# Kernel optimization log

Hardware: AMD Instinct MI355X
Metric: run time of the kernel (lower is better)

Reference implementation:

```python
import jax, jax.numpy as jnp
import numpy as np

B, T, C, H = 2, 2048, 1024, 16
D = C // H  # head_dim = 64


def wheel_softmax(scores):
    """Wheel-arithmetic softmax: total division, bot (0/0) positions -> 0.
    Rows that are entirely -inf yield sum==0 -> bot -> filled with 0.0,
    matching wheel_out.to_numpy_safe(bot_fill=0.0, inf_fill=0.0)."""
    m = jnp.max(scores, axis=-1, keepdims=True)
    safe_m = jnp.where(jnp.isfinite(m), m, 0.0)
    e = jnp.exp(scores - safe_m)          # -inf entries -> 0
    z = jnp.sum(e, axis=-1, keepdims=True)
    ok = z > 0
    return jnp.where(ok, e / jnp.where(ok, z, 1.0), 0.0)


def setup_inputs() -> dict:
    key = jax.random.key(0)
    ks = jax.random.split(key, 12)
    s = 1.0 / np.sqrt(C)
    inp = {
        "query": jax.random.normal(ks[0], (B, T, C), jnp.float32),
        "key": jax.random.normal(ks[1], (B, T, C), jnp.float32),
        "value": jax.random.normal(ks[2], (B, T, C), jnp.float32),
        "q_w": jax.random.normal(ks[3], (C, C), jnp.float32) * s,
        "q_b": jax.random.normal(ks[4], (C,), jnp.float32) * 0.01,
        "k_w": jax.random.normal(ks[5], (C, C), jnp.float32) * s,
        "k_b": jax.random.normal(ks[6], (C,), jnp.float32) * 0.01,
        "v_w": jax.random.normal(ks[7], (C, C), jnp.float32) * s,
        "v_b": jax.random.normal(ks[8], (C,), jnp.float32) * 0.01,
        "o_w": jax.random.normal(ks[9], (C, C), jnp.float32) * s,
        "o_b": jax.random.normal(ks[10], (C,), jnp.float32) * 0.01,
        "key_padding_mask": jax.random.randint(ks[11], (B, T), 0, 2).astype(bool),
    }
    return inp


def reference(query, key, value, q_w, q_b, k_w, k_b, v_w, v_b, o_w, o_b, key_padding_mask):
    scale = D ** -0.5
    def proj(x, w, b):
        # nn.Linear: x @ w.T + b ; reshape to [B,H,T,D]
        y = jnp.einsum("btc,oc->bto", x, w) + b
        return y.reshape(B, T, H, D).transpose(0, 2, 1, 3)
    Q = proj(query, q_w, q_b)
    K = proj(key, k_w, k_b)
    V = proj(value, v_w, v_b)
    scores = jnp.einsum("bhqd,bhkd->bhqk", Q, K) * scale
    scores = jnp.where(key_padding_mask[:, None, None, :], -jnp.inf, scores)
    weights = wheel_softmax(scores)  # dropout=0 -> identity
    out = jnp.einsum("bhqk,bhkd->bhqd", weights, V)
    out = out.transpose(0, 2, 1, 3).reshape(B, T, C)
    out = jnp.einsum("btc,oc->bto", out, o_w) + o_b
    return (out, weights)
```

## Files before the change

### kernel.cpp

```cpp
#include <hip/hip_runtime.h>
#include <math.h>


typedef _Float16 f16;
typedef _Float16 f16x2 __attribute__((ext_vector_type(2)));
typedef _Float16 f16x4 __attribute__((ext_vector_type(4)));
typedef _Float16 f16x8 __attribute__((ext_vector_type(8)));
typedef float  f32x2  __attribute__((ext_vector_type(2)));
typedef float  f32x4  __attribute__((ext_vector_type(4)));

#define MFMAH(a, b, c)  __builtin_amdgcn_mfma_f32_16x16x32_f16((a), (b), (c), 0, 0, 0)

__device__ __forceinline__ void gload16(void* lds, const void* g) {
  __builtin_amdgcn_global_load_lds((__attribute__((address_space(1))) void*)(g),
                                   (__attribute__((address_space(3))) void*)(lds),
                                   16, 0, 0);
}

__global__ __launch_bounds__(256) void conv_f16(const float* __restrict__ q, const float* __restrict__ k,
                                                const float* __restrict__ v, const float* __restrict__ qw,
                                                const float* __restrict__ kw, const float* __restrict__ vw,
                                                const float* __restrict__ ow, f16* __restrict__ xf) {
  long long i = ((long long)blockIdx.x * 256 + threadIdx.x) * 4;
  const float* src;
  long long off;
  if (i < 4194304)       { src = q;  off = 0; }
  else if (i < 8388608)  { src = k;  off = 4194304; }
  else if (i < 12582912) { src = v;  off = 8388608; }
  else if (i < 13631488) { src = qw; off = 12582912; }
  else if (i < 14680064) { src = kw; off = 13631488; }
  else if (i < 15728640) { src = vw; off = 14680064; }
  else                   { src = ow; off = 15728640; }
  f32x4 val = *(const f32x4*)(src + (i - off));
  f16x4 h;
#pragma unroll
  for (int r = 0; r < 4; ++r) h[r] = (f16)val[r];
  *(f16x4*)(xf + i) = h;
}

__device__ __forceinline__ void stage_tile(f16* lds, const f16* g, int row0, int kc, int tid) {
#pragma unroll
  for (int j = 0; j < 2; ++j) {
    int chunk = j * 256 + tid;
    int r = chunk >> 2, cpos = chunk & 3;
    int csrc = cpos ^ ((r >> 1) & 3);
    gload16((char*)lds + chunk * 16,
            (const char*)(g + (size_t)(row0 + r) * 1024 + kc) + csrc * 16);
  }
}

__device__ __forceinline__ f16x8 frag_ld(const f16* lds, int row, int g) {
  int pos = g ^ ((row >> 1) & 3);
  return *(const f16x8*)((const char*)lds + row * 64 + pos * 16);
}

__device__ __forceinline__ void gemm_core(const f16* A, const f16* X, int o0, int t0, int tid,
                                          f16* sA, f16* sB, f32x4 acc[4][4]) {
  int wid = tid >> 6, lane = tid & 63;
  int wm = wid >> 1, wn = wid & 1, g = lane >> 4, r15 = lane & 15;
  for (int kc = 0; kc < 1024; kc += 32) {
    __syncthreads();
    stage_tile(sA, A, o0, kc, tid);
    stage_tile(sB, X, t0, kc, tid);
    __syncthreads();
    f16x8 a[4], x[4];
#pragma unroll
    for (int f = 0; f < 4; ++f) {
      a[f] = frag_ld(sA, wm * 64 + f * 16 + r15, g);
      x[f] = frag_ld(sB, wn * 64 + f * 16 + r15, g);
    }
#pragma unroll
    for (int fm = 0; fm < 4; ++fm)
#pragma unroll
      for (int fn = 0; fn < 4; ++fn)
        acc[fm][fn] = MFMAH(a[fm], x[fn], acc[fm][fn]);
  }
}

__global__ __launch_bounds__(256) void gemm_qk(const f16* __restrict__ xf,
                                               const float* __restrict__ q_b, const float* __restrict__ k_b,
                                               f16* __restrict__ Qf, f16* __restrict__ Kf) {
  __shared__ f16 sA[4096], sB[4096];
  int z = blockIdx.z;
  const f16* A = xf + (z ? 13631488 : 12582912);
  const f16* X = xf + (z ? 4194304 : 0);
  const float* bias = z ? k_b : q_b;
  f16* Yf = z ? Kf : Qf;
  float scale = z ? 1.0f : 0.125f;
  int tid = threadIdx.x;
  int o0 = blockIdx.x * 128, t0 = blockIdx.y * 128;
  int wid = tid >> 6, lane = tid & 63;
  int wm = wid >> 1, wn = wid & 1, g = lane >> 4, r15 = lane & 15;
  f32x4 acc[4][4] = {};
  gemm_core(A, X, o0, t0, tid, sA, sB, acc);
#pragma unroll
  for (int fm = 0; fm < 4; ++fm)
#pragma unroll
    for (int fn = 0; fn < 4; ++fn) {
      int ob = o0 + wm * 64 + fm * 16 + 4 * g;
      int t  = t0 + wn * 64 + fn * 16 + r15;
      int bb = t >> 11, tl = t & 2047, hh = ob >> 6, dd = ob & 63;
      size_t base = (((size_t)bb * 16 + hh) * 2048 + tl) * 64 + dd;
      f16x4 vh;
#pragma unroll
      for (int r = 0; r < 4; ++r)
        vh[r] = (f16)((acc[fm][fn][r] + bias[ob + r]) * scale);
      *(f16x4*)(Yf + base) = vh;
    }
}

__global__ __launch_bounds__(256) void gemm_v(const f16* __restrict__ xf,
                                              const float* __restrict__ bias, f16* __restrict__ VT2) {
  __shared__ f16 sA[4096], sB[4096];
  const f16* X = xf + 8388608;
  const f16* W = xf + 14680064;
  int tid = threadIdx.x;
  int t0 = blockIdx.x * 128, o0 = blockIdx.y * 128;
  int wid = tid >> 6, lane = tid & 63;
  int wm = wid >> 1, wn = wid & 1, g = lane >> 4, r15 = lane & 15;
  f32x4 acc[4][4] = {};
  gemm_core(X, W, t0, o0, tid, sA, sB, acc);
#pragma unroll
  for (int fm = 0; fm < 4; ++fm)
#pragma unroll
    for (int fn = 0; fn < 4; ++fn) {
      int tb = t0 + wm * 64 + fm * 16 + 4 * g;
      int o  = o0 + wn * 64 + fn * 16 + r15;
      int bb = tb >> 11, tl = tb & 2047, hh = o >> 6, dd = o & 63;
      int ch = tl >> 5, c = tl & 31;
      int slotbase = (c < 16) ? ((c >> 2) << 3) : ((((c - 16) >> 2) << 3) + 4);
      float bo = bias[o];
      f16x4 v4;
#pragma unroll
      for (int r = 0; r < 4; ++r) v4[r] = (f16)(acc[fm][fn][r] + bo);
      *(f16x4*)(VT2 + ((((size_t)bb * 16 + hh) * 64 + ch) * 64 + dd) * 32 + slotbase) = v4;
    }
}

__global__ __launch_bounds__(256) void gemm_o(const f16* __restrict__ xf, const f16* __restrict__ Abuf,
                                              const float* __restrict__ o_b, float* __restrict__ OutF) {
  __shared__ f16 sA[4096], sB[4096];
  const f16* A = xf + 15728640;
  int tid = threadIdx.x;
  int o0 = blockIdx.x * 128, t0 = blockIdx.y * 128;
  int wid = tid >> 6, lane = tid & 63;
  int wm = wid >> 1, wn = wid & 1, g = lane >> 4, r15 = lane & 15;
  f32x4 acc[4][4] = {};
  gemm_core(A, Abuf, o0, t0, tid, sA, sB, acc);
#pragma unroll
  for (int fm = 0; fm < 4; ++fm)
#pragma unroll
    for (int fn = 0; fn < 4; ++fn) {
      int ob = o0 + wm * 64 + fm * 16 + 4 * g;
      int t  = t0 + wn * 64 + fn * 16 + r15;
      f32x4 v;
#pragma unroll
      for (int r = 0; r < 4; ++r) v[r] = acc[fm][fn][r] + o_b[ob + r];
      *(f32x4*)(OutF + (size_t)t * 1024 + ob) = v;
    }
}

__global__ __launch_bounds__(512, 4) void attn_kernel(
    const f16* __restrict__ Qf, const f16* __restrict__ Kf,
    const f16* __restrict__ VT2, const int* __restrict__ mask,
    float* __restrict__ wout, f16* __restrict__ Abuf) {
  __shared__ f16 kstage[8][2][1024];
  __shared__ float pvbuf[8 * 1088];
  __shared__ float ps[128];
  __shared__ float rz[16];
  int tid = threadIdx.x;
  int wid = tid >> 6, lane = tid & 63;
  int g = lane >> 4, r15 = lane & 15;
  int qt = blockIdx.x & 127, bh = blockIdx.x >> 7;
  int b = bh >> 4, h = bh & 15;
  int q0 = qt * 16;

  const f16* qp = Qf + ((size_t)bh * 2048 + q0 + r15) * 64 + 8 * g;
  f16x8 qh0 = *(const f16x8*)(qp);
  f16x8 qh1 = *(const f16x8*)(qp + 32);

  const int* mp = mask + b * 2048 + wid * 256 + 4 * g;
  unsigned long long mb = 0;
#pragma unroll
  for (int t = 0; t < 16; ++t) {
    int4 ma = *(const int4*)(mp + t * 16);
    mb |= ((ma.x ? 1ull : 0ull) << (4 * t)) | ((ma.y ? 1ull : 0ull) << (4 * t + 1)) |
          ((ma.z ? 1ull : 0ull) << (4 * t + 2)) | ((ma.w ? 1ull : 0ull) << (4 * t + 3));
  }

  f16* kb0 = &kstage[wid][0][0];
  f16* kb1 = &kstage[wid][1][0];
  const f16* ksrcA = Kf + ((size_t)bh * 2048 + wid * 256 + (lane >> 3)) * 64 +
                     (((lane & 7) ^ ((lane >> 3) & 7)) * 8);
  const f16* ksrcB = ksrcA + 8 * 64;

  gload16(kb0, ksrcA);
  gload16(kb0 + 512, ksrcB);
  gload16(kb1, ksrcA + 1024);
  gload16(kb1 + 512, ksrcB + 1024);

  float psum = 0.f;
  f16x4 p16[16];
  int key = r15 & 7;
#pragma unroll
  for (int s = 0; s < 16; ++s) {
    if (s < 15) {
      asm volatile("s_waitcnt vmcnt(2)" ::: "memory");
    } else {
      asm volatile("s_waitcnt vmcnt(0)" ::: "memory");
    }
    const f16* kt = (s & 1) ? kb1 : kb0;
    f16x8 c0 = *(const f16x8*)(kt + r15 * 64 + ((g ^ key) * 8));
    f16x8 c1 = *(const f16x8*)(kt + r15 * 64 + (((g + 4) ^ key) * 8));
    asm volatile("s_waitcnt lgkmcnt(0)" ::: "memory");
    if (s < 14) {
      f16* nb = (s & 1) ? kb1 : kb0;
      gload16(nb, ksrcA + (s + 2) * 1024);
      gload16(nb + 512, ksrcB + (s + 2) * 1024);
    }
    f32x4 sc = {0.f, 0.f, 0.f, 0.f};
    sc = MFMAH(c0, qh0, sc);
    sc = MFMAH(c1, qh1, sc);
    f16x4 pk;
#pragma unroll
    for (int r = 0; r < 4; ++r) {
      float e = ((mb >> (4 * s + r)) & 1) ? 0.f : __expf(sc[r]);
      psum += e;
      pk[r] = (f16)e;
    }
    p16[s] = pk;
  }

  psum += __shfl_xor(psum, 16);
  psum += __shfl_xor(psum, 32);
  if (lane < 16) ps[lane * 8 + wid] = psum;
  __syncthreads();

  if (tid < 128) {
    float z = ps[tid];
#pragma unroll
    for (int m = 1; m <= 4; m <<= 1) z += __shfl_xor(z, m);
    if ((tid & 7) == 0) rz[tid >> 3] = (z > 0.f) ? 1.0f / z : 0.0f;
  }
  __syncthreads();

  f32x4 acc[4] = {};
  {
    float rzv = rz[r15];
    float* wb = wout + ((size_t)bh * 2048 + q0 + r15) * 2048 + wid * 256 + 4 * g;
    const f16* vb = VT2 + (((size_t)bh * 64 + wid * 8) * 64 + r15) * 32 + g * 8;
    f16x8 v0 = *(const f16x8*)(vb);
    f16x8 v1 = *(const f16x8*)(vb + 512);
    f16x8 v2 = *(const f16x8*)(vb + 1024);
    f16x8 v3 = *(const f16x8*)(vb + 1536);
#pragma unroll
    for (int t = 0; t < 8; ++t) {
      f16x8 n0, n1, n2, n3;
      if (t < 7) {
        const f16* nvb = vb + (t + 1) * 2048;
        n0 = *(const f16x8*)(nvb);
        n1 = *(const f16x8*)(nvb + 512);
        n2 = *(const f16x8*)(nvb + 1024);
        n3 = *(const f16x8*)(nvb + 1536);
      }
#pragma unroll
      for (int u = 0; u < 2; ++u) {
        int s = 2 * t + u;
        f16x4 pk = p16[s];
        f32x4 wv;
#pragma unroll
        for (int r = 0; r < 4; ++r) wv[r] = (float)pk[r] * rzv;
        __builtin_nontemporal_store(wv, (f32x4*)(wb + s * 16));
      }
      f16x8 af = __builtin_shufflevector(p16[2 * t], p16[2 * t + 1], 0, 1, 2, 3, 4, 5, 6, 7);
      acc[0] = MFMAH(af, v0, acc[0]);
      acc[1] = MFMAH(af, v1, acc[1]);
      acc[2] = MFMAH(af, v2, acc[2]);
      acc[3] = MFMAH(af, v3, acc[3]);
      v0 = n0; v1 = n1; v2 = n2; v3 = n3;
    }
#pragma unroll
    for (int dt = 0; dt < 4; ++dt)
#pragma unroll
      for (int r = 0; r < 4; ++r)
        pvbuf[wid * 1088 + (4 * g + r) * 68 + dt * 16 + r15] = acc[dt][r];
  }
  __syncthreads();

  {
    int q = tid >> 5, d = (tid & 31) * 2;
    float a0 = 0.f, a1 = 0.f;
#pragma unroll
    for (int w8 = 0; w8 < 8; ++w8) {
      f32x2 v = *(const f32x2*)&pvbuf[w8 * 1088 + q * 68 + d];
      a0 += v[0];
      a1 += v[1];
    }
    float rzq = rz[q];
    f16x2 o2 = {(f16)(a0 * rzq), (f16)(a1 * rzq)};
    *(f16x2*)(Abuf + ((size_t)b * 2048 + q0 + q) * 1024 + h * 64 + d) = o2;
  }
}

extern "C" void kernel_launch(void* const* d_in, const int* in_sizes, int n_in,
                              void* d_out, int out_size, void* d_ws, size_t ws_size,
                              hipStream_t stream) {
  const float* query = (const float*)d_in[0];
  const float* key_i = (const float*)d_in[1];
  const float* value = (const float*)d_in[2];
  const float* q_w = (const float*)d_in[3];
  const float* q_b = (const float*)d_in[4];
  const float* k_w = (const float*)d_in[5];
  const float* k_b = (const float*)d_in[6];
  const float* v_w = (const float*)d_in[7];
  const float* v_b = (const float*)d_in[8];
  const float* o_w = (const float*)d_in[9];
  const float* o_b = (const float*)d_in[10];
  const int* mask = (const int*)d_in[11];
  float* out = (float*)d_out;
  float* wout = out + 4194304;

  const size_t XFB = 16777216ull * 2;
  const size_t QB = 4194304ull * 2;
  if (ws_size < XFB + 2 * QB) return;
  f16* xf = (f16*)d_ws;
  f16* Qf = (f16*)((char*)d_ws + XFB);
  f16* Kf = (f16*)((char*)d_ws + XFB + QB);
  f16* VT2 = xf;
  f16* Abuf = xf + 4194304;

  conv_f16<<<16384, 256, 0, stream>>>(query, key_i, value, q_w, k_w, v_w, o_w, xf);
  gemm_qk<<<dim3(8, 32, 2), 256, 0, stream>>>(xf, q_b, k_b, Qf, Kf);
  gemm_v<<<dim3(32, 8), 256, 0, stream>>>(xf, v_b, VT2);
  attn_kernel<<<4096, 512, 0, stream>>>(Qf, Kf, VT2, mask, wout, Abuf);
  gemm_o<<<dim3(8, 32), 256, 0, stream>>>(xf, Abuf, o_b, out);
}
```

Baseline: 264.2 us.

## Merge QKV projection launches, prefetch K fragments, use f16 PV partials

Combines the Q/K and V projection GEMMs into one launch with a z==2 branch, moving VT2 and Abuf to dedicated workspace regions so the merged kernel does not overwrite its own inputs. In attention, the K-fragment LDS reads are software-pipelined one step ahead of the MFMAs. The cross-wave P·V partial buffer is stored in f16 to cut LDS footprint and traffic, and odd blocks sleep briefly to stagger startup. The f16 partials reduce precision, and the larger workspace requirement may cause an early return if the workspace is too small.

```diff
diff --git a/kernel.cpp b/kernel.cpp
--- a/kernel.cpp
+++ b/kernel.cpp
@@ -77,64 +77,60 @@
   }
 }
 
-__global__ __launch_bounds__(256) void gemm_qk(const f16* __restrict__ xf,
-                                               const float* __restrict__ q_b, const float* __restrict__ k_b,
-                                               f16* __restrict__ Qf, f16* __restrict__ Kf) {
+__global__ __launch_bounds__(256) void gemm_qkv(const f16* __restrict__ xf,
+                                                const float* __restrict__ q_b, const float* __restrict__ k_b,
+                                                const float* __restrict__ v_b,
+                                                f16* __restrict__ Qf, f16* __restrict__ Kf,
+                                                f16* __restrict__ VT2) {
   __shared__ f16 sA[4096], sB[4096];
   int z = blockIdx.z;
-  const f16* A = xf + (z ? 13631488 : 12582912);
-  const f16* X = xf + (z ? 4194304 : 0);
-  const float* bias = z ? k_b : q_b;
-  f16* Yf = z ? Kf : Qf;
-  float scale = z ? 1.0f : 0.125f;
   int tid = threadIdx.x;
-  int o0 = blockIdx.x * 128, t0 = blockIdx.y * 128;
   int wid = tid >> 6, lane = tid & 63;
   int wm = wid >> 1, wn = wid & 1, g = lane >> 4, r15 = lane & 15;
   f32x4 acc[4][4] = {};
-  gemm_core(A, X, o0, t0, tid, sA, sB, acc);
-#pragma unroll
-  for (int fm = 0; fm < 4; ++fm)
-#pragma unroll
-    for (int fn = 0; fn < 4; ++fn) {
-      int ob = o0 + wm * 64 + fm * 16 + 4 * g;
-      int t  = t0 + wn * 64 + fn * 16 + r15;
-      int bb = t >> 11, tl = t & 2047, hh = ob >> 6, dd = ob & 63;
-      size_t base = (((size_t)bb * 16 + hh) * 2048 + tl) * 64 + dd;
-      f16x4 vh;
-#pragma unroll
-      for (int r = 0; r < 4; ++r)
-        vh[r] = (f16)((acc[fm][fn][r] + bias[ob + r]) * scale);
-      *(f16x4*)(Yf + base) = vh;
-    }
-}
-
-__global__ __launch_bounds__(256) void gemm_v(const f16* __restrict__ xf,
-                                              const float* __restrict__ bias, f16* __restrict__ VT2) {
-  __shared__ f16 sA[4096], sB[4096];
-  const f16* X = xf + 8388608;
-  const f16* W = xf + 14680064;
-  int tid = threadIdx.x;
-  int t0 = blockIdx.x * 128, o0 = blockIdx.y * 128;
-  int wid = tid >> 6, lane = tid & 63;
-  int wm = wid >> 1, wn = wid & 1, g = lane >> 4, r15 = lane & 15;
-  f32x4 acc[4][4] = {};
-  gemm_core(X, W, t0, o0, tid, sA, sB, acc);
-#pragma unroll
-  for (int fm = 0; fm < 4; ++fm)
-#pragma unroll
-    for (int fn = 0; fn < 4; ++fn) {
-      int tb = t0 + wm * 64 + fm * 16 + 4 * g;
-      int o  = o0 + wn * 64 + fn * 16 + r15;
-      int bb = tb >> 11, tl = tb & 2047, hh = o >> 6, dd = o & 63;
-      int ch = tl >> 5, c = tl & 31;
-      int slotbase = (c < 16) ? ((c >> 2) << 3) : ((((c - 16) >> 2) << 3) + 4);
-      float bo = bias[o];
-      f16x4 v4;
-#pragma unroll
-      for (int r = 0; r < 4; ++r) v4[r] = (f16)(acc[fm][fn][r] + bo);
-      *(f16x4*)(VT2 + ((((size_t)bb * 16 + hh) * 64 + ch) * 64 + dd) * 32 + slotbase) = v4;
-    }
+  if (z == 2) {
+    const f16* X = xf + 8388608;
+    const f16* W = xf + 14680064;
+    int o0 = blockIdx.x * 128, t0 = blockIdx.y * 128;
+    gemm_core(X, W, t0, o0, tid, sA, sB, acc);
+#pragma unroll
+    for (int fm = 0; fm < 4; ++fm)
+#pragma unroll
+      for (int fn = 0; fn < 4; ++fn) {
+        int tb = t0 + wm * 64 + fm * 16 + 4 * g;
+        int o  = o0 + wn * 64 + fn * 16 + r15;
+        int bb = tb >> 11, tl = tb & 2047, hh = o >> 6, dd = o & 63;
+        int ch = tl >> 5, c = tl & 31;
+        int slotbase = (c < 16) ? ((c >> 2) << 3) : ((((c - 16) >> 2) << 3) + 4);
+        float bo = v_b[o];
+        f16x4 v4;
+#pragma unroll
+        for (int r = 0; r < 4; ++r) v4[r] = (f16)(acc[fm][fn][r] + bo);
+        *(f16x4*)(VT2 + ((((size_t)bb * 16 + hh) * 64 + ch) * 64 + dd) * 32 + slotbase) = v4;
+      }
+  } else {
+    const f16* A = xf + (z ? 13631488 : 12582912);
+    const f16* X = xf + (z ? 4194304 : 0);
+    const float* bias = z ? k_b : q_b;
+    f16* Yf = z ? Kf : Qf;
+    float scale = z ? 1.0f : 0.125f;
+    int o0 = blockIdx.x * 128, t0 = blockIdx.y * 128;
+    gemm_core(A, X, o0, t0, tid, sA, sB, acc);
+#pragma unroll
+    for (int fm = 0; fm < 4; ++fm)
+#pragma unroll
+      for (int fn = 0; fn < 4; ++fn) {
+        int ob = o0 + wm * 64 + fm * 16 + 4 * g;
+        int t  = t0 + wn * 64 + fn * 16 + r15;
+        int bb = t >> 11, tl = t & 2047, hh = ob >> 6, dd = ob & 63;
+        size_t base = (((size_t)bb * 16 + hh) * 2048 + tl) * 64 + dd;
+        f16x4 vh;
+#pragma unroll
+        for (int r = 0; r < 4; ++r)
+          vh[r] = (f16)((acc[fm][fn][r] + bias[ob + r]) * scale);
+        *(f16x4*)(Yf + base) = vh;
+      }
+  }
 }
 
 __global__ __launch_bounds__(256) void gemm_o(const f16* __restrict__ xf, const f16* __restrict__ Abuf,
@@ -165,7 +161,7 @@
     const f16* __restrict__ VT2, const int* __restrict__ mask,
     float* __restrict__ wout, f16* __restrict__ Abuf) {
   __shared__ f16 kstage[8][2][1024];
-  __shared__ float pvbuf[8 * 1088];
+  __shared__ f16 pvh[8][16][72];
   __shared__ float ps[128];
   __shared__ float rz[16];
   int tid = threadIdx.x;
@@ -175,6 +171,8 @@
   int b = bh >> 4, h = bh & 15;
   int q0 = qt * 16;
 
+  if (blockIdx.x & 1) __builtin_amdgcn_s_sleep(24);
+
   const f16* qp = Qf + ((size_t)bh * 2048 + q0 + r15) * 64 + 8 * g;
   f16x8 qh0 = *(const f16x8*)(qp);
   f16x8 qh1 = *(const f16x8*)(qp + 32);
@@ -198,25 +196,28 @@
   gload16(kb0 + 512, ksrcB);
   gload16(kb1, ksrcA + 1024);
   gload16(kb1 + 512, ksrcB + 1024);
+  asm volatile("s_waitcnt vmcnt(2)" ::: "memory");
+  int key = r15 & 7;
+  f16x8 c0 = *(const f16x8*)(kb0 + r15 * 64 + ((g ^ key) * 8));
+  f16x8 c1 = *(const f16x8*)(kb0 + r15 * 64 + (((g + 4) ^ key) * 8));
 
   float psum = 0.f;
   f16x4 p16[16];
-  int key = r15 & 7;
 #pragma unroll
   for (int s = 0; s < 16; ++s) {
-    if (s < 15) {
-      asm volatile("s_waitcnt vmcnt(2)" ::: "memory");
-    } else {
-      asm volatile("s_waitcnt vmcnt(0)" ::: "memory");
-    }
-    const f16* kt = (s & 1) ? kb1 : kb0;
-    f16x8 c0 = *(const f16x8*)(kt + r15 * 64 + ((g ^ key) * 8));
-    f16x8 c1 = *(const f16x8*)(kt + r15 * 64 + (((g + 4) ^ key) * 8));
-    asm volatile("s_waitcnt lgkmcnt(0)" ::: "memory");
     if (s < 14) {
+      asm volatile("s_waitcnt lgkmcnt(0)" ::: "memory");
       f16* nb = (s & 1) ? kb1 : kb0;
       gload16(nb, ksrcA + (s + 2) * 1024);
       gload16(nb + 512, ksrcB + (s + 2) * 1024);
+    }
+    f16x8 n0, n1;
+    if (s < 15) {
+      if (s < 14) asm volatile("s_waitcnt vmcnt(2)" ::: "memory");
+      else        asm volatile("s_waitcnt vmcnt(0)" ::: "memory");
+      const f16* nt = ((s + 1) & 1) ? kb1 : kb0;
+      n0 = *(const f16x8*)(nt + r15 * 64 + ((g ^ key) * 8));
+      n1 = *(const f16x8*)(nt + r15 * 64 + (((g + 4) ^ key) * 8));
     }
     f32x4 sc = {0.f, 0.f, 0.f, 0.f};
     sc = MFMAH(c0, qh0, sc);
@@ -229,6 +230,8 @@
       pk[r] = (f16)e;
     }
     p16[s] = pk;
+    c0 = n0;
+    c1 = n1;
   }
 
   psum += __shfl_xor(psum, 16);
@@ -283,7 +286,7 @@
     for (int dt = 0; dt < 4; ++dt)
 #pragma unroll
       for (int r = 0; r < 4; ++r)
-        pvbuf[wid * 1088 + (4 * g + r) * 68 + dt * 16 + r15] = acc[dt][r];
+        pvh[wid][4 * g + r][dt * 16 + r15] = (f16)acc[dt][r];
   }
   __syncthreads();
 
@@ -292,9 +295,9 @@
     float a0 = 0.f, a1 = 0.f;
 #pragma unroll
     for (int w8 = 0; w8 < 8; ++w8) {
-      f32x2 v = *(const f32x2*)&pvbuf[w8 * 1088 + q * 68 + d];
-      a0 += v[0];
-      a1 += v[1];
+      f16x2 v = *(const f16x2*)&pvh[w8][q][d];
+      a0 += (float)v[0];
+      a1 += (float)v[1];
     }
     float rzq = rz[q];
     f16x2 o2 = {(f16)(a0 * rzq), (f16)(a1 * rzq)};
@@ -328,10 +331,13 @@
   f16* Kf = (f16*)((char*)d_ws + XFB + QB);
   f16* VT2 = xf;
   f16* Abuf = xf + 4194304;
+  VT2 = (f16*)((char*)d_ws + XFB + 2 * QB - 0);
+  VT2  = (f16*)((char*)d_ws + XFB + 2 * QB);
+  Abuf = (f16*)((char*)d_ws + XFB + 3 * QB);
+  if (ws_size < XFB + 4 * QB) return;
 
   conv_f16<<<16384, 256, 0, stream>>>(query, key_i, value, q_w, k_w, v_w, o_w, xf);
-  gemm_qk<<<dim3(8, 32, 2), 256, 0, stream>>>(xf, q_b, k_b, Qf, Kf);
-  gemm_v<<<dim3(32, 8), 256, 0, stream>>>(xf, v_b, VT2);
+  gemm_qkv<<<dim3(8, 32, 3), 256, 0, stream>>>(xf, q_b, k_b, v_b, Qf, Kf, VT2);
   attn_kernel<<<4096, 512, 0, stream>>>(Qf, Kf, VT2, mask, wout, Abuf);
   gemm_o<<<dim3(8, 32), 256, 0, stream>>>(xf, Abuf, o_b, out);
 }
```

New measurement: 264.2 us. About the same (+0.0%).
